# Kernel optimization log

Hardware: AMD Instinct MI355X
Metric: run time of the kernel (lower is better)

Reference implementation:

```python
import jax, jax.numpy as jnp
import numpy as np

E = 1024      # embed_dim
H = 16        # num heads
D = E // H    # head_dim = 64
B, T = 4, 2048


def setup_inputs() -> dict:
    key = jax.random.key(0)
    ks = jax.random.split(key, 7)
    hidden_states = jax.random.normal(ks[0], (B, T, E), dtype=jnp.float32)
    # torch Linear weight layout: [out_features, in_features]
    Wqkv = jax.random.normal(ks[1], (3 * E, E), dtype=jnp.float32) * (1.0 / np.sqrt(E))
    bqkv = jax.random.normal(ks[2], (3 * E,), dtype=jnp.float32) * 0.02
    Wproj = jax.random.normal(ks[3], (E, E), dtype=jnp.float32) * (1.0 / np.sqrt(E))
    bproj = jax.random.normal(ks[4], (E,), dtype=jnp.float32) * 0.02
    splat_scale = jax.random.normal(ks[5], (H,), dtype=jnp.float32) * 0.5
    splat_bias = jax.random.normal(ks[6], (H, 1, 1), dtype=jnp.float32) * 0.5
    return {
        'hidden_states': hidden_states,
        'Wqkv': Wqkv, 'bqkv': bqkv,
        'Wproj': Wproj, 'bproj': bproj,
        'splat_scale': splat_scale, 'splat_bias': splat_bias,
    }


def reference(hidden_states, Wqkv, bqkv, Wproj, bproj, splat_scale, splat_bias):
    b, t, _ = hidden_states.shape
    scale_factor = 1.0 / np.sqrt(D)

    qkv = hidden_states @ Wqkv.T + bqkv                    # [B,T,3E]
    q, k, v = jnp.split(qkv, 3, axis=-1)
    # [B,H,T,D]
    q = q.reshape(b, t, H, D).transpose(0, 2, 1, 3)
    k = k.reshape(b, t, H, D).transpose(0, 2, 1, 3)
    v = v.reshape(b, t, H, D).transpose(0, 2, 1, 3)

    scores = jnp.einsum('bhqd,bhkd->bhqk', q * scale_factor, k)  # [B,H,T,T]

    s = (1.0 + 0.01 * jnp.tanh(splat_scale)).reshape(1, H, 1, 1)
    bsp = (0.001 * jnp.tanh(splat_bias)).reshape(1, H, 1, 1)
    scores = s * scores + bsp

    causal = jnp.tril(jnp.ones((t, t), dtype=bool))
    scores = jnp.where(causal, scores, jnp.float32(-1e9))

    attn = jax.nn.softmax(scores, axis=-1)                 # dropout = identity (eval)
    out = jnp.einsum('bhqk,bhkd->bhqd', attn, v)
    out = out.transpose(0, 2, 1, 3).reshape(b, t, E)
    out = out @ Wproj.T + bproj
    return out
```

## Files before the change

kernel.cpp:

```cpp
#include <hip/hip_runtime.h>
#include <stdint.h>

#define BB 4
#define TT 2048
#define EE 1024
#define HH 16
#define DD 64
#define MM (BB*TT)
#define NQKV (3*EE)

typedef __bf16 bf16_t;
typedef bf16_t bf16x8 __attribute__((ext_vector_type(8)));
typedef short  s16x4  __attribute__((ext_vector_type(4)));
typedef float  floatx4 __attribute__((ext_vector_type(4)));

__device__ __forceinline__ unsigned short f2bf(float f) {
    unsigned int u = __float_as_uint(f);
    u = (u + 0x7FFFu + ((u >> 16) & 1u)) >> 16;
    return (unsigned short)u;
}

__device__ __forceinline__ void load_lds16(const void* g, void* l) {
    __builtin_amdgcn_global_load_lds(
        (const __attribute__((address_space(1))) unsigned int*)g,
        (__attribute__((address_space(3))) unsigned int*)l, 16, 0, 0);
}

__global__ void cvt_f32_bf16(const float* __restrict__ in,
                             unsigned short* __restrict__ out, int n) {
    int i = (blockIdx.x * 256 + threadIdx.x) * 4;
    if (i + 3 < n) {
        float4 v = *reinterpret_cast<const float4*>(in + i);
        ushort4 o;
        o.x = f2bf(v.x); o.y = f2bf(v.y); o.z = f2bf(v.z); o.w = f2bf(v.w);
        *reinterpret_cast<ushort4*>(out + i) = o;
    }
}

template<int N, int K, int EPI>
__global__ __launch_bounds__(256, 3) void gemm_bt(
    const unsigned short* __restrict__ A,
    const unsigned short* __restrict__ Bw,
    const float* __restrict__ bias,
    const float* __restrict__ sscale,
    unsigned short* __restrict__ Qb,
    unsigned short* __restrict__ Kb,
    unsigned short* __restrict__ Vtb,
    float* __restrict__ Cout)
{
    __shared__ __align__(16) unsigned short As[2][128 * 32];
    __shared__ __align__(16) unsigned short Bs[2][128 * 32];
    __shared__ float qsc[16];

    const int tid  = threadIdx.x;
    const int lane = tid & 63;
    const int w    = tid >> 6;
    const int quad = lane >> 4;
    const int l16  = lane & 15;
    const int m0   = blockIdx.y * 128;
    const int n0   = blockIdx.x * 128;
    const int wm   = (w & 1) * 64;
    const int wn   = (w >> 1) * 64;

    if (EPI == 0 && tid < 16) qsc[tid] = (1.0f + 0.01f * tanhf(sscale[tid])) * 0.125f;

    floatx4 acc[4][4] = {};

    for (int kk = 0; kk < K; kk += 64) {
        __syncthreads();
#pragma unroll
        for (int h = 0; h < 2; ++h) {
#pragma unroll
            for (int c = 0; c < 2; ++c) {
                int idx = c * 256 + tid;
                const unsigned short* ga = A  + (size_t)(m0 + (idx >> 2)) * K + kk + h * 32 + (idx & 3) * 8;
                load_lds16(ga, &As[h][(c * 256 + w * 64) * 8]);
                const unsigned short* gb = Bw + (size_t)(n0 + (idx >> 2)) * K + kk + h * 32 + (idx & 3) * 8;
                load_lds16(gb, &Bs[h][(c * 256 + w * 64) * 8]);
            }
        }
        __syncthreads();

#pragma unroll
        for (int h = 0; h < 2; ++h) {
            bf16x8 af[4], bfr[4];
#pragma unroll
            for (int mt = 0; mt < 4; ++mt)
                af[mt] = *reinterpret_cast<const bf16x8*>(&As[h][(wm + mt * 16 + l16) * 32 + quad * 8]);
#pragma unroll
            for (int nt = 0; nt < 4; ++nt)
                bfr[nt] = *reinterpret_cast<const bf16x8*>(&Bs[h][(wn + nt * 16 + l16) * 32 + quad * 8]);
#pragma unroll
            for (int mt = 0; mt < 4; ++mt)
#pragma unroll
                for (int nt = 0; nt < 4; ++nt)
                    acc[mt][nt] = __builtin_amdgcn_mfma_f32_16x16x32_bf16(af[mt], bfr[nt], acc[mt][nt], 0, 0, 0);
        }
    }

    if (EPI == 0) {
#pragma unroll
        for (int mt = 0; mt < 4; ++mt) {
            int rowb = m0 + wm + mt * 16 + quad * 4;
#pragma unroll
            for (int nt = 0; nt < 4; ++nt) {
                int col = n0 + wn + nt * 16 + l16;
                int which = col >> 10;
                int e = col & 1023;
                int h = e >> 6, d = e & 63;
                float bsv = bias[col];
#pragma unroll
                for (int r = 0; r < 4; ++r) {
                    int m = rowb + r;
                    int b = m >> 11, t = m & 2047;
                    float v = acc[mt][nt][r] + bsv;
                    size_t bh = (size_t)(b * HH + h);
                    if (which == 0) {
                        v *= qsc[h];
                        Qb[(bh * TT + t) * DD + d] = f2bf(v);
                    } else if (which == 1) {
                        Kb[(bh * TT + t) * DD + d] = f2bf(v);
                    } else {
                        Vtb[(bh * DD + d) * TT + t] = f2bf(v);
                    }
                }
            }
        }
    } else {
#pragma unroll
        for (int mt = 0; mt < 4; ++mt) {
            int rowb = m0 + wm + mt * 16 + quad * 4;
#pragma unroll
            for (int nt = 0; nt < 4; ++nt) {
                int col = n0 + wn + nt * 16 + l16;
                float bsv = bias[col];
#pragma unroll
                for (int r = 0; r < 4; ++r)
                    Cout[(size_t)(rowb + r) * N + col] = acc[mt][nt][r] + bsv;
            }
        }
    }
}

#define LP 72
__global__ __launch_bounds__(256, 4) void flash_attn(
    const unsigned short* __restrict__ Qb,
    const unsigned short* __restrict__ Kb,
    const unsigned short* __restrict__ Vtb,
    unsigned short* __restrict__ Ob)
{
    __shared__ __align__(16) unsigned short Ks[2][64 * LP];
    __shared__ __align__(16) unsigned short Vs[2][64 * LP];

    const int tid  = threadIdx.x;
    const int lane = tid & 63;
    const int w    = tid >> 6;
    const int quad = lane >> 4;
    const int l16  = lane & 15;
    const int i    = blockIdx.x;
    const int bh   = i & 63;
    const int qt   = 31 - (i >> 6);
    const int row0 = qt * 64 + w * 16;

    const unsigned short* qbase = &Qb[((size_t)bh * TT + row0 + l16) * DD + quad * 8];
    const bf16x8 qf0 = *reinterpret_cast<const bf16x8*>(qbase);
    const bf16x8 qf1 = *reinterpret_cast<const bf16x8*>(qbase + 32);

    const s16x4 vones = { (short)0x3F80, (short)0x3F80, (short)0x3F80, (short)0x3F80 };

    floatx4 o[4] = {};
    floatx4 o1 = {};

    const int srow = tid >> 3;
    const int scol = (tid & 7) * 8;
    const size_t kgbase = ((size_t)bh * TT + srow) * DD + scol;
    const size_t vgbase = ((size_t)bh * DD + srow) * TT + scol;

    uint4 kr0 = *reinterpret_cast<const uint4*>(&Kb[kgbase]);
    uint4 kr1 = *reinterpret_cast<const uint4*>(&Kb[kgbase + 32 * DD]);
    uint4 vr0 = *reinterpret_cast<const uint4*>(&Vtb[vgbase]);
    uint4 vr1 = *reinterpret_cast<const uint4*>(&Vtb[vgbase + 32 * TT]);

    for (int kt = 0; kt <= qt; ++kt) {
        const int buf = kt & 1;
        *reinterpret_cast<uint4*>(&Ks[buf][srow * LP + scol]) = kr0;
        *reinterpret_cast<uint4*>(&Ks[buf][(srow + 32) * LP + scol]) = kr1;
        *reinterpret_cast<uint4*>(&Vs[buf][srow * LP + scol]) = vr0;
        *reinterpret_cast<uint4*>(&Vs[buf][(srow + 32) * LP + scol]) = vr1;
        __syncthreads();

        if (kt < qt) {
            size_t ko = kgbase + (size_t)(kt + 1) * 64 * DD;
            size_t vo = vgbase + (size_t)(kt + 1) * 64;
            kr0 = *reinterpret_cast<const uint4*>(&Kb[ko]);
            kr1 = *reinterpret_cast<const uint4*>(&Kb[ko + 32 * DD]);
            vr0 = *reinterpret_cast<const uint4*>(&Vtb[vo]);
            vr1 = *reinterpret_cast<const uint4*>(&Vtb[vo + 32 * TT]);
        }

        const int keyb = kt * 64 + quad * 4;
        const int qr0  = row0 + l16;
        const bool diag = (kt == qt);

#pragma unroll
        for (int ntk = 0; ntk < 4; ++ntk) {
            const unsigned short* krow = &Ks[buf][(ntk * 16 + l16) * LP + quad * 8];
            bf16x8 kf0 = *reinterpret_cast<const bf16x8*>(krow);
            bf16x8 kf1 = *reinterpret_cast<const bf16x8*>(krow + 32);

            floatx4 st = {0.f, 0.f, 0.f, 0.f};
            st = __builtin_amdgcn_mfma_f32_16x16x32_bf16(kf0, qf0, st, 0, 0, 0);
            st = __builtin_amdgcn_mfma_f32_16x16x32_bf16(kf1, qf1, st, 0, 0, 0);

            s16x4 pf;
#pragma unroll
            for (int r = 0; r < 4; ++r) {
                float p = __expf(st[r]);
                pf[r] = (short)((!diag || (keyb + ntk * 16 + r <= qr0)) ? f2bf(p) : 0);
            }

            o1 = __builtin_amdgcn_mfma_f32_16x16x16bf16_1k(pf, vones, o1, 0, 0, 0);
#pragma unroll
            for (int dt = 0; dt < 4; ++dt) {
                s16x4 vf = *reinterpret_cast<const s16x4*>(
                    &Vs[buf][(dt * 16 + l16) * LP + ntk * 16 + quad * 4]);
                o[dt] = __builtin_amdgcn_mfma_f32_16x16x16bf16_1k(pf, vf, o[dt], 0, 0, 0);
            }
        }
    }

    const int b = bh >> 4, h = bh & 15;
#pragma unroll
    for (int r = 0; r < 4; ++r) {
        int q = row0 + quad * 4 + r;
        float rl = __builtin_amdgcn_rcpf(o1[r]);
#pragma unroll
        for (int dt = 0; dt < 4; ++dt)
            Ob[((size_t)(b * TT + q)) * EE + h * DD + dt * 16 + l16] =
                f2bf(o[dt][r] * rl);
    }
}

extern "C" void kernel_launch(void* const* d_in, const int* in_sizes, int n_in,
                              void* d_out, int out_size, void* d_ws, size_t ws_size,
                              hipStream_t stream) {
    const float* hs    = (const float*)d_in[0];
    const float* Wqkv  = (const float*)d_in[1];
    const float* bqkv  = (const float*)d_in[2];
    const float* Wproj = (const float*)d_in[3];
    const float* bproj = (const float*)d_in[4];
    const float* ss    = (const float*)d_in[5];
    float* out = (float*)d_out;

    char* p = (char*)d_ws;
    unsigned short* hsb    = (unsigned short*)p; p += (size_t)MM * EE * 2;
    unsigned short* wqkvb  = (unsigned short*)p; p += (size_t)NQKV * EE * 2;
    unsigned short* wprojb = (unsigned short*)p; p += (size_t)EE * EE * 2;
    unsigned short* Qb     = (unsigned short*)p; p += (size_t)BB*HH*TT*DD * 2;
    unsigned short* Kb     = (unsigned short*)p; p += (size_t)BB*HH*TT*DD * 2;
    unsigned short* Vtb    = (unsigned short*)p; p += (size_t)BB*HH*TT*DD * 2;

    cvt_f32_bf16<<<(MM * EE) / 1024, 256, 0, stream>>>(hs, hsb, MM * EE);
    cvt_f32_bf16<<<(NQKV * EE) / 1024, 256, 0, stream>>>(Wqkv, wqkvb, NQKV * EE);
    cvt_f32_bf16<<<(EE * EE) / 1024, 256, 0, stream>>>(Wproj, wprojb, EE * EE);

    gemm_bt<NQKV, EE, 0><<<dim3(NQKV / 128, MM / 128), 256, 0, stream>>>(
        hsb, wqkvb, bqkv, ss, Qb, Kb, Vtb, nullptr);

    flash_attn<<<dim3(2048), 256, 0, stream>>>(Qb, Kb, Vtb, hsb);

    gemm_bt<EE, EE, 1><<<dim3(EE / 128, MM / 128), 256, 0, stream>>>(
        hsb, wprojb, bproj, nullptr, nullptr, nullptr, nullptr, out);
}
```

Measured before the change: 281.1 us.

## Replace GEMM with 256x256 tile, 512-thread, multi-stage pipelined MFMA kernel

Replaces the 128x128 double-buffered GEMM with a 256x256 tile kernel using 8 waves, a 4-slot LDS ring, and prefetch issued two k-steps ahead. Loads are interleaved with MFMA blocks, waits use explicit vmcnt and barriers, and MFMA sections run at raised wave priority. Workgroup indices are remapped across XCDs for locality. This targets global-load latency and per-k-step sync overhead in both the QKV and output projections, at the cost of more registers (an 8x4 accumulator) and a K=1024 value hardcoded into the loop structure.

Measured after the change: 307.4 us. +9.3%, slower.

```diff
diff --git a/kernel.cpp b/kernel.cpp
--- a/kernel.cpp
+++ b/kernel.cpp
@@ -37,8 +37,54 @@
     }
 }
 
-template<int N, int K, int EPI>
-__global__ __launch_bounds__(256, 3) void gemm_bt(
+#define VW(N) asm volatile("s_waitcnt vmcnt(" #N ")" ::: "memory")
+#define BARX() do { __builtin_amdgcn_s_barrier(); asm volatile("" ::: "memory"); } while (0)
+#define FR(p, t) (*reinterpret_cast<const bf16x8*>((p) + (t) * 512))
+#define MFMA1(mi, ni, av, bv) \
+    acc[mi][ni] = __builtin_amdgcn_mfma_f32_16x16x32_bf16(av, bv, acc[mi][ni], 0, 0, 0)
+#define MFMA_BLK(M0) do { \
+    MFMA1(M0+0,0,a0,b0); MFMA1(M0+0,1,a0,b1); MFMA1(M0+0,2,a0,b2); MFMA1(M0+0,3,a0,b3); \
+    MFMA1(M0+1,0,a1,b0); MFMA1(M0+1,1,a1,b1); MFMA1(M0+1,2,a1,b2); MFMA1(M0+1,3,a1,b3); \
+    MFMA1(M0+2,0,a2,b0); MFMA1(M0+2,1,a2,b1); MFMA1(M0+2,2,a2,b2); MFMA1(M0+2,3,a2,b3); \
+    MFMA1(M0+3,0,a3,b0); MFMA1(M0+3,1,a3,b1); MFMA1(M0+3,2,a3,b2); MFMA1(M0+3,3,a3,b3); \
+} while (0)
+#define STEP_A(kt_, h_) do { \
+    const unsigned short* _g = Ag + (kt_) * 64 + (h_) * 32; \
+    unsigned short* _l = (unsigned short*)&As[(2*(kt_)+(h_)) & 3][w * 512]; \
+    load_lds16(_g, _l); \
+    load_lds16(_g + (size_t)128 * 1024, _l + 4096); \
+} while (0)
+#define STEP_B(kt_, h_) do { \
+    const unsigned short* _g = Bg + (kt_) * 64 + (h_) * 32; \
+    unsigned short* _l = (unsigned short*)&Bs[(2*(kt_)+(h_)) & 3][w * 512]; \
+    load_lds16(_g, _l); \
+    load_lds16(_g + (size_t)128 * 1024, _l + 4096); \
+} while (0)
+#define TILE_BODY(kt_, W1CODE, W3CODE, DOISS) do { \
+    const int _s0 = (2 * (kt_)) & 3; \
+    const unsigned short* _ap0 = &As[_s0][aoff]; \
+    const unsigned short* _bp0 = &Bs[_s0][boff]; \
+    const unsigned short* _ap1 = &As[_s0 + 1][aoff]; \
+    const unsigned short* _bp1 = &Bs[_s0 + 1][boff]; \
+    bf16x8 a0, a1, a2, a3, b0, b1, b2, b3; \
+    a0 = FR(_ap0, 0); a1 = FR(_ap0, 1); a2 = FR(_ap0, 2); a3 = FR(_ap0, 3); \
+    b0 = FR(_bp0, 0); b1 = FR(_bp0, 1); b2 = FR(_bp0, 2); b3 = FR(_bp0, 3); \
+    BARX(); __builtin_amdgcn_s_setprio(1); MFMA_BLK(0); __builtin_amdgcn_s_setprio(0); BARX(); \
+    a0 = FR(_ap0, 4); a1 = FR(_ap0, 5); a2 = FR(_ap0, 6); a3 = FR(_ap0, 7); \
+    BARX(); __builtin_amdgcn_s_setprio(1); MFMA_BLK(4); __builtin_amdgcn_s_setprio(0); W1CODE; BARX(); \
+    a0 = FR(_ap1, 0); a1 = FR(_ap1, 1); a2 = FR(_ap1, 2); a3 = FR(_ap1, 3); \
+    b0 = FR(_bp1, 0); b1 = FR(_bp1, 1); b2 = FR(_bp1, 2); b3 = FR(_bp1, 3); \
+    BARX(); __builtin_amdgcn_s_setprio(1); \
+    if (DOISS) { STEP_A((kt_) + 2, 0); STEP_B((kt_) + 2, 0); } \
+    MFMA_BLK(0); __builtin_amdgcn_s_setprio(0); BARX(); \
+    a0 = FR(_ap1, 4); a1 = FR(_ap1, 5); a2 = FR(_ap1, 6); a3 = FR(_ap1, 7); \
+    BARX(); __builtin_amdgcn_s_setprio(1); \
+    if (DOISS) { STEP_A((kt_) + 2, 1); STEP_B((kt_) + 2, 1); } \
+    MFMA_BLK(4); __builtin_amdgcn_s_setprio(0); W3CODE; BARX(); \
+} while (0)
+
+template<int N, int EPI>
+__global__ __launch_bounds__(512, 2) void gemm256(
     const unsigned short* __restrict__ A,
     const unsigned short* __restrict__ Bw,
     const float* __restrict__ bias,
@@ -48,76 +94,67 @@
     unsigned short* __restrict__ Vtb,
     float* __restrict__ Cout)
 {
-    __shared__ __align__(16) unsigned short As[2][128 * 32];
-    __shared__ __align__(16) unsigned short Bs[2][128 * 32];
-    __shared__ float qsc[16];
+    __shared__ __align__(16) unsigned short As[4][8192];
+    __shared__ __align__(16) unsigned short Bs[4][8192];
 
     const int tid  = threadIdx.x;
     const int lane = tid & 63;
     const int w    = tid >> 6;
     const int quad = lane >> 4;
     const int l16  = lane & 15;
-    const int m0   = blockIdx.y * 128;
-    const int n0   = blockIdx.x * 128;
-    const int wm   = (w & 1) * 64;
-    const int wn   = (w >> 1) * 64;
-
-    if (EPI == 0 && tid < 16) qsc[tid] = (1.0f + 0.01f * tanhf(sscale[tid])) * 0.125f;
-
-    floatx4 acc[4][4] = {};
-
-    for (int kk = 0; kk < K; kk += 64) {
-        __syncthreads();
-#pragma unroll
-        for (int h = 0; h < 2; ++h) {
-#pragma unroll
-            for (int c = 0; c < 2; ++c) {
-                int idx = c * 256 + tid;
-                const unsigned short* ga = A  + (size_t)(m0 + (idx >> 2)) * K + kk + h * 32 + (idx & 3) * 8;
-                load_lds16(ga, &As[h][(c * 256 + w * 64) * 8]);
-                const unsigned short* gb = Bw + (size_t)(n0 + (idx >> 2)) * K + kk + h * 32 + (idx & 3) * 8;
-                load_lds16(gb, &Bs[h][(c * 256 + w * 64) * 8]);
-            }
-        }
-        __syncthreads();
-
-#pragma unroll
-        for (int h = 0; h < 2; ++h) {
-            bf16x8 af[4], bfr[4];
-#pragma unroll
-            for (int mt = 0; mt < 4; ++mt)
-                af[mt] = *reinterpret_cast<const bf16x8*>(&As[h][(wm + mt * 16 + l16) * 32 + quad * 8]);
-#pragma unroll
-            for (int nt = 0; nt < 4; ++nt)
-                bfr[nt] = *reinterpret_cast<const bf16x8*>(&Bs[h][(wn + nt * 16 + l16) * 32 + quad * 8]);
-#pragma unroll
-            for (int mt = 0; mt < 4; ++mt)
-#pragma unroll
-                for (int nt = 0; nt < 4; ++nt)
-                    acc[mt][nt] = __builtin_amdgcn_mfma_f32_16x16x32_bf16(af[mt], bfr[nt], acc[mt][nt], 0, 0, 0);
-        }
-    }
+
+    const int nwg = (int)gridDim.x;
+    const int wg  = ((int)blockIdx.x & 7) * (nwg >> 3) + ((int)blockIdx.x >> 3);
+    const int nbx = N / 256;
+    const int m0  = (wg / nbx) * 256;
+    const int n0  = (wg % nbx) * 256;
+
+    const int wm = (w >> 2) * 128;
+    const int wn = (w & 3) * 64;
+
+    const int srow = tid >> 2;
+    const int scol = (tid & 3) * 8;
+    const unsigned short* Ag = A  + (size_t)(m0 + srow) * 1024 + scol;
+    const unsigned short* Bg = Bw + (size_t)(n0 + srow) * 1024 + scol;
+
+    const int aoff = (wm + l16) * 32 + quad * 8;
+    const int boff = (wn + l16) * 32 + quad * 8;
+
+    floatx4 acc[8][4] = {};
+
+    STEP_A(0, 0); STEP_B(0, 0); STEP_A(0, 1); STEP_B(0, 1);
+    STEP_A(1, 0); STEP_B(1, 0); STEP_A(1, 1); STEP_B(1, 1);
+    VW(12); BARX();
+
+#pragma unroll 2
+    for (int kt = 0; kt < 14; ++kt) {
+        TILE_BODY(kt, VW(8), VW(12), 1);
+    }
+    TILE_BODY(14, VW(8), VW(4), 0);
+    TILE_BODY(15, VW(0), (void)0, 0);
 
     if (EPI == 0) {
-#pragma unroll
-        for (int mt = 0; mt < 4; ++mt) {
-            int rowb = m0 + wm + mt * 16 + quad * 4;
-#pragma unroll
-            for (int nt = 0; nt < 4; ++nt) {
-                int col = n0 + wn + nt * 16 + l16;
-                int which = col >> 10;
-                int e = col & 1023;
-                int h = e >> 6, d = e & 63;
-                float bsv = bias[col];
+        const int colb  = n0 + wn;
+        const int which = colb >> 10;
+#pragma unroll
+        for (int nt = 0; nt < 4; ++nt) {
+            const int col = colb + nt * 16 + l16;
+            const int e = col & 1023;
+            const int hh = e >> 6, d = e & 63;
+            const float bsv = bias[col];
+            float qs = 0.f;
+            if (which == 0) qs = (1.0f + 0.01f * tanhf(sscale[hh])) * 0.125f;
+#pragma unroll
+            for (int mt = 0; mt < 8; ++mt) {
+                const int rowb = m0 + wm + mt * 16 + quad * 4;
 #pragma unroll
                 for (int r = 0; r < 4; ++r) {
-                    int m = rowb + r;
-                    int b = m >> 11, t = m & 2047;
+                    const int m = rowb + r;
+                    const int b = m >> 11, t = m & 2047;
+                    const size_t bh = (size_t)(b * HH + hh);
                     float v = acc[mt][nt][r] + bsv;
-                    size_t bh = (size_t)(b * HH + h);
                     if (which == 0) {
-                        v *= qsc[h];
-                        Qb[(bh * TT + t) * DD + d] = f2bf(v);
+                        Qb[(bh * TT + t) * DD + d] = f2bf(v * qs);
                     } else if (which == 1) {
                         Kb[(bh * TT + t) * DD + d] = f2bf(v);
                     } else {
@@ -128,12 +165,12 @@
         }
     } else {
 #pragma unroll
-        for (int mt = 0; mt < 4; ++mt) {
-            int rowb = m0 + wm + mt * 16 + quad * 4;
+        for (int mt = 0; mt < 8; ++mt) {
+            const int rowb = m0 + wm + mt * 16 + quad * 4;
 #pragma unroll
             for (int nt = 0; nt < 4; ++nt) {
-                int col = n0 + wn + nt * 16 + l16;
-                float bsv = bias[col];
+                const int col = n0 + wn + nt * 16 + l16;
+                const float bsv = bias[col];
 #pragma unroll
                 for (int r = 0; r < 4; ++r)
                     Cout[(size_t)(rowb + r) * N + col] = acc[mt][nt][r] + bsv;
@@ -264,11 +301,11 @@
     cvt_f32_bf16<<<(NQKV * EE) / 1024, 256, 0, stream>>>(Wqkv, wqkvb, NQKV * EE);
     cvt_f32_bf16<<<(EE * EE) / 1024, 256, 0, stream>>>(Wproj, wprojb, EE * EE);
 
-    gemm_bt<NQKV, EE, 0><<<dim3(NQKV / 128, MM / 128), 256, 0, stream>>>(
+    gemm256<NQKV, 0><<<dim3((MM / 256) * (NQKV / 256)), 512, 0, stream>>>(
         hsb, wqkvb, bqkv, ss, Qb, Kb, Vtb, nullptr);
 
     flash_attn<<<dim3(2048), 256, 0, stream>>>(Qb, Kb, Vtb, hsb);
 
-    gemm_bt<EE, EE, 1><<<dim3(EE / 128, MM / 128), 256, 0, stream>>>(
+    gemm256<EE, 1><<<dim3((MM / 256) * (EE / 256)), 512, 0, stream>>>(
         hsb, wprojb, bproj, nullptr, nullptr, nullptr, nullptr, out);
 }
```
